# Kernel optimization log

Hardware: AMD Instinct MI355X
Metric: run time of the kernel (lower is better)

Reference implementation:

```python
import jax, jax.numpy as jnp
import numpy as np

B, M, L, D, S = 2, 4, 1024, 256, 16
WSCALE = 0.02  # keep exp(delta*A) well-conditioned

def setup_inputs() -> dict:
    key = jax.random.key(0)
    ks = jax.random.split(key, 6)
    x = jax.random.normal(ks[0], (B, M, L, D), dtype=jnp.float32)
    v = jax.random.normal(ks[1], (B, M, L, D), dtype=jnp.float32)
    W1 = jax.random.normal(ks[2], (D, D), dtype=jnp.float32) * WSCALE
    W2 = jax.random.normal(ks[3], (D, S), dtype=jnp.float32) * WSCALE
    W3 = jax.random.normal(ks[4], (D, S), dtype=jnp.float32) * WSCALE
    A = jax.random.normal(ks[5], (D, S), dtype=jnp.float32) * WSCALE
    b1 = jnp.zeros((D,), jnp.float32)
    b2 = jnp.zeros((S,), jnp.float32)
    b3 = jnp.zeros((S,), jnp.float32)
    h = jnp.zeros((B, L, M, D, S), jnp.float32)
    return {"x": x, "v": v, "W1": W1, "b1": b1, "W2": W2, "b2": b2,
            "W3": W3, "b3": b3, "A": A, "h": h}

def reference(x, v, W1, b1, W2, b2, W3, b3, A, h):
    Bb, Mm, Ll, Dd = x.shape
    Ss = W2.shape[1]
    # projections on flattened (B*M*L, D), then reshaped to (B, L, M, .)
    # NOTE: this reinterprets the (M, L) flattening order, matching the
    # original torch code's .view(-1, D) followed by .view(B, L, M, .).
    xf = x.reshape(-1, Dd)
    vf = v.reshape(-1, Dd)
    E  = (vf @ W2 + b2).reshape(Bb, Ll, Mm, Ss)
    Bm = (xf @ W2 + b2).reshape(Bb, Ll, Mm, Ss)
    C  = (xf @ W3 + b3).reshape(Bb, Ll, Mm, Ss)
    x_fc1 = xf @ W1 + b1
    Dm = x_fc1.reshape(Bb, Ll, Mm, Dd)
    Fm = (vf @ W1 + b1).reshape(Bb, Ll, Mm, Dd)
    delta = jax.nn.softplus(x_fc1).reshape(Bb, Ll, Mm, Dd)
    # discretization: dB/dE outer products, dA = exp(delta * A)
    dB = delta[..., :, None] * Bm[..., None, :]          # (B,L,M,D,S)
    dE = delta[..., :, None] * E[..., None, :]           # (B,L,M,D,S)
    dA = jnp.exp(jnp.einsum('blmd,dn->blmdn', delta, A)) # (B,L,M,D,S)
    # state update (h is a zeros buffer in the original, never carried)
    xt = jnp.transpose(x, (0, 2, 1, 3))  # (B,L,M,D)
    vt = jnp.transpose(v, (0, 2, 1, 3))
    h_new = dA * h + xt[..., None] * dB + vt[..., None] * dE
    y = jnp.einsum('blmn,blmdn->blmd', C, h_new)
    return y * Dm + y * Fm + y
```

## Files before the change

kernel.cpp:

```cpp
#include <hip/hip_runtime.h>
#include <cmath>


#define DD 256

typedef __bf16 bf16x8 __attribute__((ext_vector_type(8)));
typedef float  f32x4  __attribute__((ext_vector_type(4)));
typedef unsigned short us8 __attribute__((ext_vector_type(8)));

static __device__ __forceinline__ float softplus_f(float x) {
    return fmaxf(x, 0.0f) + log1pf(expf(-fabsf(x)));
}

__global__ void prep_w(const float* __restrict__ W1, const float* __restrict__ W2,
                       const float* __restrict__ W3, unsigned short* __restrict__ WTf)
{
    const int tid  = blockIdx.x * 256 + threadIdx.x;
    const int lane = tid & 63;
    const int ks   = (tid >> 6) & 7;
    const int t    = tid >> 9;
    const int k0   = ks * 32 + (lane >> 4) * 8;
    const int nl   = lane & 15;
    unsigned short o[8];
    if (t < 16) {
        const int n = t * 16 + nl;
        #pragma unroll
        for (int j = 0; j < 8; ++j) {
            const __bf16 h = (__bf16)W1[(size_t)(k0 + j) * 256 + n];
            o[j] = __builtin_bit_cast(unsigned short, h);
        }
    } else {
        const float* __restrict__ W = (t == 16) ? W2 : W3;
        #pragma unroll
        for (int j = 0; j < 8; ++j) {
            const __bf16 h = (__bf16)W[(size_t)(k0 + j) * 16 + nl];
            o[j] = __builtin_bit_cast(unsigned short, h);
        }
    }
    *(us8*)(WTf + (size_t)tid * 8) = *(const us8*)o;
}

__global__ __launch_bounds__(512, 4) void s6_main(
    const float* __restrict__ x, const float* __restrict__ v,
    const unsigned short* __restrict__ WTf,
    const float* __restrict__ b1, const float* __restrict__ b2,
    const float* __restrict__ b3, float* __restrict__ out)
{
    const int w    = threadIdx.x >> 6;
    const int lane = threadIdx.x & 63;
    const int ar   = lane & 15;
    const int g    = lane >> 4;
    const int q0   = blockIdx.x * 16;
    const int T0   = w * 2;

    f32x4 aX0 = {0.f,0.f,0.f,0.f}, aX1 = {0.f,0.f,0.f,0.f};
    f32x4 aV0 = {0.f,0.f,0.f,0.f}, aV1 = {0.f,0.f,0.f,0.f};
    f32x4 aBm = {0.f,0.f,0.f,0.f}, aE  = {0.f,0.f,0.f,0.f}, aC = {0.f,0.f,0.f,0.f};

    const us8* __restrict__ fb = (const us8*)WTf;

    #pragma unroll
    for (int ks = 0; ks < 8; ++ks) {
        const size_t base = (size_t)(q0 + ar) * DD + ks * 32 + g * 8;
        const float4 x0 = *(const float4*)(x + base);
        const float4 x1 = *(const float4*)(x + base + 4);
        const float4 v0 = *(const float4*)(v + base);
        const float4 v1 = *(const float4*)(v + base + 4);
        bf16x8 axk, avk;
        axk[0] = (__bf16)x0.x; axk[1] = (__bf16)x0.y; axk[2] = (__bf16)x0.z; axk[3] = (__bf16)x0.w;
        axk[4] = (__bf16)x1.x; axk[5] = (__bf16)x1.y; axk[6] = (__bf16)x1.z; axk[7] = (__bf16)x1.w;
        avk[0] = (__bf16)v0.x; avk[1] = (__bf16)v0.y; avk[2] = (__bf16)v0.z; avk[3] = (__bf16)v0.w;
        avk[4] = (__bf16)v1.x; avk[5] = (__bf16)v1.y; avk[6] = (__bf16)v1.z; avk[7] = (__bf16)v1.w;

        const bf16x8 bf0 = __builtin_bit_cast(bf16x8, fb[((T0 + 0) * 8 + ks) * 64 + lane]);
        const bf16x8 bf1 = __builtin_bit_cast(bf16x8, fb[((T0 + 1) * 8 + ks) * 64 + lane]);
        const bf16x8 bf2 = __builtin_bit_cast(bf16x8, fb[(16 * 8 + ks) * 64 + lane]);
        const bf16x8 bf3 = __builtin_bit_cast(bf16x8, fb[(17 * 8 + ks) * 64 + lane]);

        aX0 = __builtin_amdgcn_mfma_f32_16x16x32_bf16(axk, bf0, aX0, 0, 0, 0);
        aV0 = __builtin_amdgcn_mfma_f32_16x16x32_bf16(avk, bf0, aV0, 0, 0, 0);
        aX1 = __builtin_amdgcn_mfma_f32_16x16x32_bf16(axk, bf1, aX1, 0, 0, 0);
        aV1 = __builtin_amdgcn_mfma_f32_16x16x32_bf16(avk, bf1, aV1, 0, 0, 0);
        aBm = __builtin_amdgcn_mfma_f32_16x16x32_bf16(axk, bf2, aBm, 0, 0, 0);
        aE  = __builtin_amdgcn_mfma_f32_16x16x32_bf16(avk, bf2, aE , 0, 0, 0);
        aC  = __builtin_amdgcn_mfma_f32_16x16x32_bf16(axk, bf3, aC , 0, 0, 0);
    }

    float s1j[4], s2j[4];
    {
        const float bb2 = b2[ar];
        const float bb3 = b3[ar];
        #pragma unroll
        for (int j = 0; j < 4; ++j) {
            const float C = aC[j] + bb3;
            float pb = C * (aBm[j] + bb2);
            float pe = C * (aE[j]  + bb2);
            #pragma unroll
            for (int off = 8; off >= 1; off >>= 1) {
                pb += __shfl_xor(pb, off);
                pe += __shfl_xor(pe, off);
            }
            s1j[j] = pb; s2j[j] = pe;
        }
    }

    #pragma unroll
    for (int i = 0; i < 2; ++i) {
        const f32x4& AX = i ? aX1 : aX0;
        const f32x4& AV = i ? aV1 : aV0;
        const int d = (T0 + i) * 16 + ar;
        const float bb1 = b1[d];
        #pragma unroll
        for (int j = 0; j < 4; ++j) {
            const int row = g * 4 + j;
            const int q = q0 + row;
            const float p1 = AX[j] + bb1;
            const float pv = AV[j] + bb1;
            const int bq = q >> 12, fq = q & 4095, li = fq >> 2, m = fq & 3;
            const size_t rp = ((size_t)(bq << 12) + (m << 10) + li) * DD + d;
            const float xt = x[rp];
            const float vt = v[rp];
            const float dl = softplus_f(p1);
            const float y  = dl * (xt * s1j[j] + vt * s2j[j]);
            out[(size_t)q * DD + d] = y * (1.0f + p1 + pv);
        }
    }
}

extern "C" void kernel_launch(void* const* d_in, const int* in_sizes, int n_in,
                              void* d_out, int out_size, void* d_ws, size_t ws_size,
                              hipStream_t stream) {
    const float* x  = (const float*)d_in[0];
    const float* v  = (const float*)d_in[1];
    const float* W1 = (const float*)d_in[2];
    const float* b1 = (const float*)d_in[3];
    const float* W2 = (const float*)d_in[4];
    const float* b2 = (const float*)d_in[5];
    const float* W3 = (const float*)d_in[6];
    const float* b3 = (const float*)d_in[7];
    float* out = (float*)d_out;
    unsigned short* WTf = (unsigned short*)d_ws;

    hipLaunchKernelGGL(prep_w, dim3(36), dim3(256), 0, stream, W1, W2, W3, WTf);
    hipLaunchKernelGGL(s6_main, dim3(512), dim3(512), 0, stream,
                       x, v, WTf, b1, b2, b3, out);
}
```

Baseline: 214.2 us.

## Drop weight prep kernel, swap MFMA operands for vectorized epilogue and stores

Removes the separate kernel that pre-converted and swizzled the weights to bf16, so the main kernel now reads fp32 weights directly with strided scalar loads and converts them in registers. The MFMA operands are swapped so each lane holds four consecutive output columns for one row. That lets the epilogue use float4 loads of the transposed x/v and float4 stores to out, and replaces the 16-lane shuffle reductions with two cross-group shuffles. The aim is to save a launch and get coalesced epilogue traffic, at the cost of many uncoalesced scalar weight loads and redundant bf16 conversions in every block.

```diff
diff --git a/kernel.cpp b/kernel.cpp
--- a/kernel.cpp
+++ b/kernel.cpp
@@ -6,45 +6,17 @@
 
 typedef __bf16 bf16x8 __attribute__((ext_vector_type(8)));
 typedef float  f32x4  __attribute__((ext_vector_type(4)));
-typedef unsigned short us8 __attribute__((ext_vector_type(8)));
 
 static __device__ __forceinline__ float softplus_f(float x) {
     return fmaxf(x, 0.0f) + log1pf(expf(-fabsf(x)));
 }
 
-__global__ void prep_w(const float* __restrict__ W1, const float* __restrict__ W2,
-                       const float* __restrict__ W3, unsigned short* __restrict__ WTf)
-{
-    const int tid  = blockIdx.x * 256 + threadIdx.x;
-    const int lane = tid & 63;
-    const int ks   = (tid >> 6) & 7;
-    const int t    = tid >> 9;
-    const int k0   = ks * 32 + (lane >> 4) * 8;
-    const int nl   = lane & 15;
-    unsigned short o[8];
-    if (t < 16) {
-        const int n = t * 16 + nl;
-        #pragma unroll
-        for (int j = 0; j < 8; ++j) {
-            const __bf16 h = (__bf16)W1[(size_t)(k0 + j) * 256 + n];
-            o[j] = __builtin_bit_cast(unsigned short, h);
-        }
-    } else {
-        const float* __restrict__ W = (t == 16) ? W2 : W3;
-        #pragma unroll
-        for (int j = 0; j < 8; ++j) {
-            const __bf16 h = (__bf16)W[(size_t)(k0 + j) * 16 + nl];
-            o[j] = __builtin_bit_cast(unsigned short, h);
-        }
-    }
-    *(us8*)(WTf + (size_t)tid * 8) = *(const us8*)o;
-}
-
 __global__ __launch_bounds__(512, 4) void s6_main(
     const float* __restrict__ x, const float* __restrict__ v,
-    const unsigned short* __restrict__ WTf,
-    const float* __restrict__ b1, const float* __restrict__ b2,
-    const float* __restrict__ b3, float* __restrict__ out)
+    const float* __restrict__ W1, const float* __restrict__ b1,
+    const float* __restrict__ W2, const float* __restrict__ b2,
+    const float* __restrict__ W3, const float* __restrict__ b3,
+    float* __restrict__ out)
 {
     const int w    = threadIdx.x >> 6;
     const int lane = threadIdx.x & 63;
@@ -52,78 +24,114 @@
     const int g    = lane >> 4;
     const int q0   = blockIdx.x * 16;
     const int T0   = w * 2;
+    const int q    = q0 + ar;
+
+    const int bq = q >> 12, fq = q & 4095, li = fq >> 2, m = fq & 3;
+    const size_t rp = ((size_t)(bq << 12) + (m << 10) + li) * DD;
+
+    const int n0 = T0 * 16 + g * 4;
+    const int n1 = n0 + 16;
+    const float4 xt0 = *(const float4*)(x + rp + n0);
+    const float4 vt0 = *(const float4*)(v + rp + n0);
+    const float4 xt1 = *(const float4*)(x + rp + n1);
+    const float4 vt1 = *(const float4*)(v + rp + n1);
 
     f32x4 aX0 = {0.f,0.f,0.f,0.f}, aX1 = {0.f,0.f,0.f,0.f};
     f32x4 aV0 = {0.f,0.f,0.f,0.f}, aV1 = {0.f,0.f,0.f,0.f};
     f32x4 aBm = {0.f,0.f,0.f,0.f}, aE  = {0.f,0.f,0.f,0.f}, aC = {0.f,0.f,0.f,0.f};
 
-    const us8* __restrict__ fb = (const us8*)WTf;
-
     #pragma unroll
     for (int ks = 0; ks < 8; ++ks) {
-        const size_t base = (size_t)(q0 + ar) * DD + ks * 32 + g * 8;
-        const float4 x0 = *(const float4*)(x + base);
-        const float4 x1 = *(const float4*)(x + base + 4);
-        const float4 v0 = *(const float4*)(v + base);
-        const float4 v1 = *(const float4*)(v + base + 4);
-        bf16x8 axk, avk;
-        axk[0] = (__bf16)x0.x; axk[1] = (__bf16)x0.y; axk[2] = (__bf16)x0.z; axk[3] = (__bf16)x0.w;
-        axk[4] = (__bf16)x1.x; axk[5] = (__bf16)x1.y; axk[6] = (__bf16)x1.z; axk[7] = (__bf16)x1.w;
-        avk[0] = (__bf16)v0.x; avk[1] = (__bf16)v0.y; avk[2] = (__bf16)v0.z; avk[3] = (__bf16)v0.w;
-        avk[4] = (__bf16)v1.x; avk[5] = (__bf16)v1.y; avk[6] = (__bf16)v1.z; avk[7] = (__bf16)v1.w;
+        const int k0 = ks * 32 + g * 8;
 
-        const bf16x8 bf0 = __builtin_bit_cast(bf16x8, fb[((T0 + 0) * 8 + ks) * 64 + lane]);
-        const bf16x8 bf1 = __builtin_bit_cast(bf16x8, fb[((T0 + 1) * 8 + ks) * 64 + lane]);
-        const bf16x8 bf2 = __builtin_bit_cast(bf16x8, fb[(16 * 8 + ks) * 64 + lane]);
-        const bf16x8 bf3 = __builtin_bit_cast(bf16x8, fb[(17 * 8 + ks) * 64 + lane]);
+        const size_t xb = (size_t)q * DD + k0;
+        const float4 x0 = *(const float4*)(x + xb);
+        const float4 x1 = *(const float4*)(x + xb + 4);
+        const float4 v0 = *(const float4*)(v + xb);
+        const float4 v1 = *(const float4*)(v + xb + 4);
+        bf16x8 xf, vf;
+        xf[0]=(__bf16)x0.x; xf[1]=(__bf16)x0.y; xf[2]=(__bf16)x0.z; xf[3]=(__bf16)x0.w;
+        xf[4]=(__bf16)x1.x; xf[5]=(__bf16)x1.y; xf[6]=(__bf16)x1.z; xf[7]=(__bf16)x1.w;
+        vf[0]=(__bf16)v0.x; vf[1]=(__bf16)v0.y; vf[2]=(__bf16)v0.z; vf[3]=(__bf16)v0.w;
+        vf[4]=(__bf16)v1.x; vf[5]=(__bf16)v1.y; vf[6]=(__bf16)v1.z; vf[7]=(__bf16)v1.w;
 
-        aX0 = __builtin_amdgcn_mfma_f32_16x16x32_bf16(axk, bf0, aX0, 0, 0, 0);
-        aV0 = __builtin_amdgcn_mfma_f32_16x16x32_bf16(avk, bf0, aV0, 0, 0, 0);
-        aX1 = __builtin_amdgcn_mfma_f32_16x16x32_bf16(axk, bf1, aX1, 0, 0, 0);
-        aV1 = __builtin_amdgcn_mfma_f32_16x16x32_bf16(avk, bf1, aV1, 0, 0, 0);
-        aBm = __builtin_amdgcn_mfma_f32_16x16x32_bf16(axk, bf2, aBm, 0, 0, 0);
-        aE  = __builtin_amdgcn_mfma_f32_16x16x32_bf16(avk, bf2, aE , 0, 0, 0);
-        aC  = __builtin_amdgcn_mfma_f32_16x16x32_bf16(axk, bf3, aC , 0, 0, 0);
+        const float* w1p0 = W1 + (size_t)k0 * DD + T0 * 16 + ar;
+        const float* w1p1 = w1p0 + 16;
+        const float* w2p  = W2 + (size_t)k0 * 16 + ar;
+        const float* w3p  = W3 + (size_t)k0 * 16 + ar;
+        bf16x8 wa0, wa1, wa2, wa3;
+        #pragma unroll
+        for (int j = 0; j < 8; ++j) {
+            wa0[j] = (__bf16)w1p0[(size_t)j * DD];
+            wa1[j] = (__bf16)w1p1[(size_t)j * DD];
+            wa2[j] = (__bf16)w2p[j * 16];
+            wa3[j] = (__bf16)w3p[j * 16];
+        }
+
+        aX0 = __builtin_amdgcn_mfma_f32_16x16x32_bf16(wa0, xf, aX0, 0, 0, 0);
+        aV0 = __builtin_amdgcn_mfma_f32_16x16x32_bf16(wa0, vf, aV0, 0, 0, 0);
+        aX1 = __builtin_amdgcn_mfma_f32_16x16x32_bf16(wa1, xf, aX1, 0, 0, 0);
+        aV1 = __builtin_amdgcn_mfma_f32_16x16x32_bf16(wa1, vf, aV1, 0, 0, 0);
+        aBm = __builtin_amdgcn_mfma_f32_16x16x32_bf16(wa2, xf, aBm, 0, 0, 0);
+        aE  = __builtin_amdgcn_mfma_f32_16x16x32_bf16(wa2, vf, aE , 0, 0, 0);
+        aC  = __builtin_amdgcn_mfma_f32_16x16x32_bf16(wa3, xf, aC , 0, 0, 0);
     }
 
-    float s1j[4], s2j[4];
+    float s1, s2;
     {
-        const float bb2 = b2[ar];
-        const float bb3 = b3[ar];
-        #pragma unroll
-        for (int j = 0; j < 4; ++j) {
-            const float C = aC[j] + bb3;
-            float pb = C * (aBm[j] + bb2);
-            float pe = C * (aE[j]  + bb2);
-            #pragma unroll
-            for (int off = 8; off >= 1; off >>= 1) {
-                pb += __shfl_xor(pb, off);
-                pe += __shfl_xor(pe, off);
-            }
-            s1j[j] = pb; s2j[j] = pe;
-        }
+        const float4 b2v = *(const float4*)(b2 + g * 4);
+        const float4 b3v = *(const float4*)(b3 + g * 4);
+        const float C0 = aC[0] + b3v.x, C1 = aC[1] + b3v.y;
+        const float C2 = aC[2] + b3v.z, C3 = aC[3] + b3v.w;
+        s1 = C0 * (aBm[0] + b2v.x) + C1 * (aBm[1] + b2v.y)
+           + C2 * (aBm[2] + b2v.z) + C3 * (aBm[3] + b2v.w);
+        s2 = C0 * (aE[0]  + b2v.x) + C1 * (aE[1]  + b2v.y)
+           + C2 * (aE[2]  + b2v.z) + C3 * (aE[3]  + b2v.w);
+        s1 += __shfl_xor(s1, 16); s1 += __shfl_xor(s1, 32);
+        s2 += __shfl_xor(s2, 16); s2 += __shfl_xor(s2, 32);
     }
 
-    #pragma unroll
-    for (int i = 0; i < 2; ++i) {
-        const f32x4& AX = i ? aX1 : aX0;
-        const f32x4& AV = i ? aV1 : aV0;
-        const int d = (T0 + i) * 16 + ar;
-        const float bb1 = b1[d];
-        #pragma unroll
-        for (int j = 0; j < 4; ++j) {
-            const int row = g * 4 + j;
-            const int q = q0 + row;
-            const float p1 = AX[j] + bb1;
-            const float pv = AV[j] + bb1;
-            const int bq = q >> 12, fq = q & 4095, li = fq >> 2, m = fq & 3;
-            const size_t rp = ((size_t)(bq << 12) + (m << 10) + li) * DD + d;
-            const float xt = x[rp];
-            const float vt = v[rp];
-            const float dl = softplus_f(p1);
-            const float y  = dl * (xt * s1j[j] + vt * s2j[j]);
-            out[(size_t)q * DD + d] = y * (1.0f + p1 + pv);
+    {
+        const float4 b1v = *(const float4*)(b1 + n0);
+        float4 o;
+        {
+            const float p1 = aX0[0] + b1v.x, pv = aV0[0] + b1v.x;
+            o.x = softplus_f(p1) * (xt0.x * s1 + vt0.x * s2) * (1.0f + p1 + pv);
         }
+        {
+            const float p1 = aX0[1] + b1v.y, pv = aV0[1] + b1v.y;
+            o.y = softplus_f(p1) * (xt0.y * s1 + vt0.y * s2) * (1.0f + p1 + pv);
+        }
+        {
+            const float p1 = aX0[2] + b1v.z, pv = aV0[2] + b1v.z;
+            o.z = softplus_f(p1) * (xt0.z * s1 + vt0.z * s2) * (1.0f + p1 + pv);
+        }
+        {
+            const float p1 = aX0[3] + b1v.w, pv = aV0[3] + b1v.w;
+            o.w = softplus_f(p1) * (xt0.w * s1 + vt0.w * s2) * (1.0f + p1 + pv);
+        }
+        *(float4*)(out + (size_t)q * DD + n0) = o;
+    }
+    {
+        const float4 b1v = *(const float4*)(b1 + n1);
+        float4 o;
+        {
+            const float p1 = aX1[0] + b1v.x, pv = aV1[0] + b1v.x;
+            o.x = softplus_f(p1) * (xt1.x * s1 + vt1.x * s2) * (1.0f + p1 + pv);
+        }
+        {
+            const float p1 = aX1[1] + b1v.y, pv = aV1[1] + b1v.y;
+            o.y = softplus_f(p1) * (xt1.y * s1 + vt1.y * s2) * (1.0f + p1 + pv);
+        }
+        {
+            const float p1 = aX1[2] + b1v.z, pv = aV1[2] + b1v.z;
+            o.z = softplus_f(p1) * (xt1.z * s1 + vt1.z * s2) * (1.0f + p1 + pv);
+        }
+        {
+            const float p1 = aX1[3] + b1v.w, pv = aV1[3] + b1v.w;
+            o.w = softplus_f(p1) * (xt1.w * s1 + vt1.w * s2) * (1.0f + p1 + pv);
+        }
+        *(float4*)(out + (size_t)q * DD + n1) = o;
     }
 }
 
@@ -139,9 +147,7 @@
     const float* W3 = (const float*)d_in[6];
     const float* b3 = (const float*)d_in[7];
     float* out = (float*)d_out;
-    unsigned short* WTf = (unsigned short*)d_ws;
 
-    hipLaunchKernelGGL(prep_w, dim3(36), dim3(256), 0, stream, W1, W2, W3, WTf);
     hipLaunchKernelGGL(s6_main, dim3(512), dim3(512), 0, stream,
-                       x, v, WTf, b1, b2, b3, out);
+                       x, v, W1, b1, W2, b2, W3, b3, out);
 }
```

Result: no change. 217.8 us (+1.7%).
